# Optimization experiments

Measured on AMD Instinct MI355X. Metric: run time of the kernel, lower is better.

Reference implementation:

```python
import jax, jax.numpy as jnp
import numpy as np

DIM = 256
NUM_HEADS = 8
HEAD_DIM = DIM // NUM_HEADS
CPB_HIDDEN = 512
B, N = 2, 2304
TABLE = 9025  # (2*48-1)**2


def _l2norm(t, eps=1e-12):
    # matches torch F.normalize(dim=-1): x / max(||x||, eps)
    n = jnp.sqrt(jnp.sum(t * t, axis=-1, keepdims=True))
    return t / jnp.maximum(n, eps)


def setup_inputs() -> dict:
    key = jax.random.key(0)
    ks = jax.random.split(key, 12)
    x = jax.random.normal(ks[0], (B, N, DIM), dtype=jnp.float32)
    relative_pos_index = jax.random.randint(ks[1], (N, N), 0, TABLE, dtype=jnp.int64)
    relative_coords_table = jax.random.uniform(ks[2], (TABLE, 2), dtype=jnp.float32) * 2.0 - 1.0
    seq_length_scale = jnp.ones((1,), dtype=jnp.float32) * jnp.log2(jnp.float32(N))
    padding_mask = jnp.zeros((B, N), dtype=jnp.int32)
    s = 0.02
    W_qkv = jax.random.normal(ks[3], (3 * DIM, DIM), dtype=jnp.float32) * s
    b_qkv = jnp.zeros((3 * DIM,), dtype=jnp.float32)
    # temperature init: log(exp(1/0.24) - 1) so softplus(temperature) = 1/0.24
    temperature = jnp.full((NUM_HEADS, 1, 1), float(np.log(np.expm1(1.0 / 0.24))), dtype=jnp.float32)
    query_embedding = jax.random.normal(ks[4], (NUM_HEADS, 1, HEAD_DIM), dtype=jnp.float32) * s
    W_proj = jax.random.normal(ks[5], (DIM, DIM), dtype=jnp.float32) * s
    b_proj = jnp.zeros((DIM,), dtype=jnp.float32)
    W_cpb1 = jax.random.normal(ks[6], (CPB_HIDDEN, 2), dtype=jnp.float32) * s
    b_cpb1 = jnp.zeros((CPB_HIDDEN,), dtype=jnp.float32)
    W_cpb2 = jax.random.normal(ks[7], (NUM_HEADS, CPB_HIDDEN), dtype=jnp.float32) * s
    b_cpb2 = jnp.zeros((NUM_HEADS,), dtype=jnp.float32)
    return {
        'x': x, 'relative_pos_index': relative_pos_index,
        'relative_coords_table': relative_coords_table,
        'seq_length_scale': seq_length_scale, 'padding_mask': padding_mask,
        'W_qkv': W_qkv, 'b_qkv': b_qkv, 'temperature': temperature,
        'query_embedding': query_embedding, 'W_proj': W_proj, 'b_proj': b_proj,
        'W_cpb1': W_cpb1, 'b_cpb1': b_cpb1, 'W_cpb2': W_cpb2, 'b_cpb2': b_cpb2,
    }


def reference(x, relative_pos_index, relative_coords_table, seq_length_scale,
              padding_mask, W_qkv, b_qkv, temperature, query_embedding,
              W_proj, b_proj, W_cpb1, b_cpb1, W_cpb2, b_cpb2):
    Bx, Nx, C = x.shape
    h, d = NUM_HEADS, HEAD_DIM
    # qkv projection -> (B, 3h, N, d); first h heads = q, then k, then v
    qkv = (jnp.einsum('bnc,oc->bno', x, W_qkv) + b_qkv)
    qkv = qkv.reshape(Bx, Nx, 3 * h, d).transpose(0, 2, 1, 3)
    q, k, v = qkv[:, :h], qkv[:, h:2 * h], qkv[:, 2 * h:]
    # CPB relative bias: (T,2) -> (T,h) -> (h,N,N) via gather
    hid = jax.nn.relu(relative_coords_table @ W_cpb1.T + b_cpb1)
    tab = hid @ W_cpb2.T + b_cpb2                    # (T, h)
    rel_bias = tab.T[:, relative_pos_index.reshape(-1)].reshape(h, Nx, Nx)
    # cosine-sim attention with learned query embedding + softplus temperature
    scale = jax.nn.softplus(temperature) * seq_length_scale[0]   # (h,1,1)
    qn = (_l2norm(q) + query_embedding) * scale                  # (B,h,N,d)
    kn = _l2norm(k)
    attn = jnp.einsum('bhnd,bhmd->bhnm', qn, kn) + rel_bias
    attn = jax.nn.softmax(attn, axis=-1)
    out = jnp.einsum('bhnm,bhmd->bhnd', attn, v)
    out = out.transpose(0, 2, 1, 3).reshape(Bx, Nx, C)
    out = out @ W_proj.T + b_proj
    return out
```

## Files before the change

kernel.cpp:

```cpp
#include <hip/hip_runtime.h>
#include <math.h>

#define DIMC 256
#define NHEADS 8
#define HDIM 32
#define CPBH 512
#define BB 2
#define NSEQ 2304
#define TAB 9025
#define TABP 9040
#define RTOT (BB*NHEADS*NSEQ)
#define SPLITS 4
#define MSP (NSEQ/SPLITS)
#define PBS 36
#define NCHUNK (NSEQ/32)
#define LOG2E 1.44269504088896340736f

#define IDXP_ELEMS    (NSEQ * NCHUNK * 16)
#define IDXP4_BLOCKS  (IDXP_ELEMS / 1024)
#define CPB_BLOCKS    ((TAB + 63) / 64)
#define QKV_BLOCKS    (12 * 72)

typedef unsigned short ushort;
typedef __attribute__((ext_vector_type(8))) short short8;
typedef __attribute__((ext_vector_type(4))) short short4v;
typedef __attribute__((ext_vector_type(4))) float f32x4;

#define MFMA16(a,b,c) __builtin_amdgcn_mfma_f32_16x16x32_bf16((a),(b),(c),0,0,0)

#define GL16(SRC, DST) __builtin_amdgcn_global_load_lds( \
    (const __attribute__((address_space(1))) void*)(SRC), \
    (__attribute__((address_space(3))) void*)(DST), 16, 0, 0)

__device__ __forceinline__ ushort f2bf(float x) {
  unsigned u = __float_as_uint(x);
  u += 0x7FFFu + ((u >> 16) & 1u);
  return (ushort)(u >> 16);
}
__device__ __forceinline__ float bf2f(ushort b) {
  return __uint_as_float(((unsigned)b) << 16);
}
__device__ __forceinline__ float fexp2(float x) {
#if defined(__has_builtin)
#if __has_builtin(__builtin_amdgcn_exp2f)
  return __builtin_amdgcn_exp2f(x);
#else
  return exp2f(x);
#endif
#else
  return exp2f(x);
#endif
}
__device__ __forceinline__ unsigned pack_trunc(float p0, float p1) {
  return __builtin_amdgcn_perm(__float_as_uint(p1), __float_as_uint(p0), 0x07060302u);
}
__device__ __forceinline__ void cvt8(const float* __restrict__ p, short8* hi, short8* lo) {
  float4 v0 = *(const float4*)p;
  float4 v1 = *(const float4*)(p + 4);
  float vv[8] = {v0.x, v0.y, v0.z, v0.w, v1.x, v1.y, v1.z, v1.w};
  short8 h, l;
#pragma unroll
  for (int i = 0; i < 8; ++i) {
    ushort hh = f2bf(vv[i]);
    h[i] = (short)hh;
    l[i] = (short)f2bf(vv[i] - bf2f(hh));
  }
  *hi = h; *lo = l;
}

__launch_bounds__(256)
__global__ void pre_kernel(const float* __restrict__ x, const float* __restrict__ wq,
                           const int* __restrict__ idx,
                           const float* __restrict__ tbl, const float* __restrict__ W1,
                           const float* __restrict__ b1, const float* __restrict__ W2,
                           const float* __restrict__ b2,
                           const float* __restrict__ bias, const float* __restrict__ temp,
                           const float* __restrict__ sls, const float* __restrict__ qe,
                           ushort* __restrict__ qhi, ushort* __restrict__ qlo,
                           ushort* __restrict__ khi, ushort* __restrict__ klo,
                           ushort* __restrict__ vT,
                           unsigned* __restrict__ idxP, ushort* __restrict__ tabBf) {
  __shared__ __align__(16) float smem[8192];
  int blk = blockIdx.x;
  int tid = threadIdx.x;

  if (blk < CPB_BLOCKS) {
    float* w1b = smem;
    float* w2t = smem + 2048;
    float* part = smem + 6144;
    for (int i = tid; i < CPBH; i += 256) {
      w1b[i * 4 + 0] = W1[2 * i];
      w1b[i * 4 + 1] = W1[2 * i + 1];
      w1b[i * 4 + 2] = b1[i];
      w1b[i * 4 + 3] = 0.f;
    }
    for (int i = tid; i < CPBH * NHEADS; i += 256)
      w2t[(i & (CPBH - 1)) * NHEADS + (i >> 9)] = W2[i];
    int tl = tid & 63, jc = tid >> 6;
    int t = blk * 64 + tl;
    bool valid = t < TAB;
    float c0 = 0.f, c1 = 0.f;
    if (valid) { c0 = tbl[2 * t]; c1 = tbl[2 * t + 1]; }
    __syncthreads();
    float acc[NHEADS];
#pragma unroll
    for (int h = 0; h < NHEADS; ++h) acc[h] = 0.f;
    for (int j = jc * 128; j < jc * 128 + 128; ++j) {
      float4 wv = *(const float4*)&w1b[j * 4];
      float hid = fmaxf(fmaf(c0, wv.x, fmaf(c1, wv.y, wv.z)), 0.f);
      float4 wa = *(const float4*)&w2t[j * NHEADS];
      float4 wb = *(const float4*)&w2t[j * NHEADS + 4];
      acc[0] = fmaf(hid, wa.x, acc[0]);
      acc[1] = fmaf(hid, wa.y, acc[1]);
      acc[2] = fmaf(hid, wa.z, acc[2]);
      acc[3] = fmaf(hid, wa.w, acc[3]);
      acc[4] = fmaf(hid, wb.x, acc[4]);
      acc[5] = fmaf(hid, wb.y, acc[5]);
      acc[6] = fmaf(hid, wb.z, acc[6]);
      acc[7] = fmaf(hid, wb.w, acc[7]);
    }
#pragma unroll
    for (int h = 0; h < NHEADS; ++h) part[((size_t)jc * 64 + tl) * NHEADS + h] = acc[h];
    __syncthreads();
    if (jc == 0 && valid) {
#pragma unroll
      for (int h = 0; h < NHEADS; ++h) {
        float s = b2[h];
#pragma unroll
        for (int p = 0; p < 4; ++p) s += part[((size_t)p * 64 + tl) * NHEADS + h];
        tabBf[h * TABP + t] = f2bf(s * LOG2E);
      }
    }
  } else if (blk < CPB_BLOCKS + QKV_BLOCKS) {
    float (*vbuf)[65] = (float(*)[65])smem;
    int t = blk - CPB_BLOCKS;
    int n0 = (t % 12) * 64, m0 = (t / 12) * 64;
    int lane = tid & 63, w = tid >> 6;
    int g = lane >> 4, c = lane & 15;
    int mw = m0 + w * 16;
    const int K = DIMC;
    f32x4 acc[4] = {{0,0,0,0},{0,0,0,0},{0,0,0,0},{0,0,0,0}};
#pragma unroll 2
    for (int k0 = 0; k0 < K; k0 += 32) {
      short8 ah, al;
      cvt8(&x[(size_t)(mw + c) * K + k0 + g * 8], &ah, &al);
#pragma unroll
      for (int nt = 0; nt < 4; ++nt) {
        short8 bh, bl;
        cvt8(&wq[(size_t)(n0 + nt * 16 + c) * K + k0 + g * 8], &bh, &bl);
        acc[nt] = MFMA16(ah, bh, acc[nt]);
        acc[nt] = MFMA16(al, bh, acc[nt]);
        acc[nt] = MFMA16(ah, bl, acc[nt]);
      }
    }
#pragma unroll
    for (int nt = 0; nt < 4; ++nt) {
      float bv = bias[n0 + nt * 16 + c];
#pragma unroll
      for (int r = 0; r < 4; ++r) acc[nt][r] += bv;
    }

    int b = (m0 >= NSEQ) ? 1 : 0;
    int nb = m0 - b * NSEQ;
    int sect = n0 >> 8;
    int hloc = (n0 & 255) >> 5;

    if (sect < 2) {
#pragma unroll
      for (int H = 0; H < 2; ++H) {
        int head = hloc + H;
        float scale = (sect == 0) ? log1pf(expf(temp[head])) * sls[0] * LOG2E : 0.f;
#pragma unroll
        for (int r = 0; r < 4; ++r) {
          float ss = acc[2*H][r]*acc[2*H][r] + acc[2*H+1][r]*acc[2*H+1][r];
          ss += __shfl_xor(ss, 1);
          ss += __shfl_xor(ss, 2);
          ss += __shfl_xor(ss, 4);
          ss += __shfl_xor(ss, 8);
          float inv = 1.f / fmaxf(sqrtf(ss), 1e-12f);
#pragma unroll
          for (int half = 0; half < 2; ++half) {
            int d = half * 16 + c;
            float val = acc[2*H + half][r] * inv;
            if (sect == 0) val = (val + qe[head * HDIM + d]) * scale;
            vbuf[w * 16 + g * 4 + r][H * 32 + d] = val;
          }
        }
      }
      __syncthreads();
      int plane = tid >> 7;
      int seg = tid & 127;
      int head = seg >> 6, row = seg & 63;
      const float* srcrow = &vbuf[row][head * 32];
      ushort out16[32];
#pragma unroll
      for (int i = 0; i < 32; ++i) {
        float v = srcrow[i];
        ushort hh = f2bf(v);
        out16[i] = plane ? f2bf(v - bf2f(hh)) : hh;
      }
      ushort* dstp = plane ? (sect == 0 ? qlo : klo) : (sect == 0 ? qhi : khi);
      size_t off = ((size_t)(b * NHEADS + hloc + head) * NSEQ + nb + row) * HDIM;
#pragma unroll
      for (int q4 = 0; q4 < 4; ++q4)
        *(int4*)&dstp[off + q4 * 8] = ((int4*)out16)[q4];
    } else {
#pragma unroll
      for (int nt = 0; nt < 4; ++nt)
#pragma unroll
        for (int r = 0; r < 4; ++r)
          vbuf[w * 16 + g * 4 + r][nt * 16 + c] = acc[nt][r];
      __syncthreads();
      int hbase = (n0 - 512) >> 5;
#pragma unroll
      for (int it = 0; it < 16; ++it) {
        int dloc = (tid >> 6) * 16 + it;
        int p = tid & 63;
        int pp = p & 31;
        int nsrc = (p & 32) + (pp & 1) * 16 + (pp >> 1);
        float v = vbuf[nsrc][dloc];
        int head = hbase + (dloc >> 5), d = dloc & 31;
        vT[((size_t)((b * NHEADS + head) * HDIM + d)) * NSEQ + nb + p] = f2bf(v);
      }
    }
  } else {
    int t4 = (blk - CPB_BLOCKS - QKV_BLOCKS) * 256 + tid;
    int grp = t4 >> 4;
    int ch = grp % NCHUNK;
    int n4 = grp / NCHUNK;
    int m = ch * 32 + (t4 & 15);
    unsigned o[4];
#pragma unroll
    for (int i = 0; i < 4; ++i) {
      unsigned lo = (unsigned)idx[(size_t)(n4 * 4 + i) * NSEQ + m];
      unsigned hi = (unsigned)idx[(size_t)(n4 * 4 + i) * NSEQ + m + 16];
      o[i] = lo | (hi << 16);
    }
    *(uint4*)&idxP[(size_t)t4 * 4] = *(const uint4*)o;
  }
}

__launch_bounds__(256)
__global__ void attn_kernel(const ushort* __restrict__ qhi, const ushort* __restrict__ qlo,
                            const ushort* __restrict__ khi, const ushort* __restrict__ klo,
                            const ushort* __restrict__ vT, const ushort* __restrict__ tabBf,
                            const unsigned* __restrict__ idxP,
                            float* __restrict__ pO, float* __restrict__ pL) {
  __shared__ ushort tbf[10240];
  __shared__ __align__(16) ushort pbuf[8][16 * PBS];
  __shared__ __align__(16) ushort stg[2][6144];
  int tid = threadIdx.x;
  int lane = tid & 63;
  int w = tid >> 6;

  int bid = blockIdx.x;
  int qb = bid >> 5;
  int k8 = bid & 7;
  int j4 = (bid >> 3) & 3;
  int y  = k8 + 8 * j4;
  int s = y & 3, h = y >> 2;

  const ushort* tsrc = tabBf + h * TABP;
#pragma unroll
  for (int i = 0; i < 5; ++i) {
    int off = i * 2048 + tid * 8;
    *(int4*)&tbf[off] = *(const int4*)&tsrc[off];
  }

  int g = lane >> 4, c = lane & 15;
  int q0 = qb * 64 + w * 16;
  int qg0 = q0 >> 2;
  size_t rowA = (size_t)h * NSEQ;
  size_t rowB = (size_t)(NHEADS + h) * NSEQ;
  int m0 = s * MSP;

  int su   = tid & 127;
  int srow = su & 31;
  int sslt = su >> 5;
  const ushort* kb0 = (tid < 128) ? khi : klo;
  const ushort* sA = kb0 + (rowA + m0 + srow) * HDIM + sslt * 8;
  const ushort* sB = kb0 + (rowB + m0 + srow) * HDIM + sslt * 8;
  const ushort* sV = vT + ((size_t)(((tid < 128) ? h : NHEADS + h) * HDIM + srow)) * NSEQ
                     + m0 + sslt * 8;
  unsigned dwb = (unsigned)(tid & 192) * 8;

#define STAGE(DP) do {                         \
    GL16(sA, (DP) + dwb);                      \
    GL16(sB, (DP) + 2048 + dwb);               \
    GL16(sV, (DP) + 4096 + dwb);               \
    sA += 32 * HDIM; sB += 32 * HDIM; sV += 32; \
  } while (0)

  short8 qAh = *(const short8*)&qhi[(rowA + q0 + c) * HDIM + g * 8];
  short8 qAl = *(const short8*)&qlo[(rowA + q0 + c) * HDIM + g * 8];
  short8 qBh = *(const short8*)&qhi[(rowB + q0 + c) * HDIM + g * 8];
  short8 qBl = *(const short8*)&qlo[(rowB + q0 + c) * HDIM + g * 8];

  unsigned oIb = (unsigned)(((unsigned)(qg0 + g) * NCHUNK + (m0 >> 5)) * 64 + c * 4);
  unsigned oI  = oIb;
  uint4 ia = *(const uint4*)&idxP[oI];

  STAGE(&stg[0][0]);
  __syncthreads();

  short one = (c == 0) ? (short)0x3F80 : (short)0;
  short8 onesB = {one, one, one, one, one, one, one, one};

  f32x4 oa0 = {0,0,0,0}, oa1 = {0,0,0,0}, ob0 = {0,0,0,0}, ob1 = {0,0,0,0};
  f32x4 la = {0,0,0,0}, lb = {0,0,0,0};
  ushort* pba = pbuf[w * 2];
  ushort* pbb = pbuf[w * 2 + 1];

  int kbo = g * 256 + c * 8;
  int cur = 0;

  for (int mt = m0; mt < m0 + MSP; mt += 32) {
    bool lastit = (mt + 32 >= m0 + MSP);
    unsigned oIn = lastit ? oIb : oI + 64;
    uint4 ian = *(const uint4*)&idxP[oIn];
    oI = oIn;
    if (!lastit) STAGE(&stg[cur ^ 1][0]);

    const ushort* S = &stg[cur][0];
    short8 ak0h = *(const short8*)&S[kbo];
    short8 ak1h = *(const short8*)&S[kbo + 128];
    short8 ak0l = *(const short8*)&S[1024 + kbo];
    short8 ak1l = *(const short8*)&S[1024 + kbo + 128];
    short8 bk0h = *(const short8*)&S[2048 + kbo];
    short8 bk1h = *(const short8*)&S[2048 + kbo + 128];
    short8 bk0l = *(const short8*)&S[3072 + kbo];
    short8 bk1l = *(const short8*)&S[3072 + kbo + 128];

    f32x4 sa0 = {0,0,0,0}, sa1 = {0,0,0,0}, sb0 = {0,0,0,0}, sb1 = {0,0,0,0};
    sa0 = MFMA16(qAh, ak0h, sa0);
    sa1 = MFMA16(qAh, ak1h, sa1);
    sb0 = MFMA16(qBh, bk0h, sb0);
    sb1 = MFMA16(qBh, bk1h, sb1);
    sa0 = MFMA16(qAl, ak0h, sa0);
    sa1 = MFMA16(qAl, ak1h, sa1);
    sb0 = MFMA16(qBl, bk0h, sb0);
    sb1 = MFMA16(qBl, bk1h, sb1);
    sa0 = MFMA16(qAh, ak0l, sa0);
    sa1 = MFMA16(qAh, ak1l, sa1);
    sb0 = MFMA16(qBh, bk0l, sb0);
    sb1 = MFMA16(qBh, bk1l, sb1);

    unsigned ip[4] = {ia.x, ia.y, ia.z, ia.w};
    float b0[4], b1[4];
#pragma unroll
    for (int r = 0; r < 4; ++r) {
      b0[r] = bf2f(tbf[ip[r] & 0xFFFF]);
      b1[r] = bf2f(tbf[ip[r] >> 16]);
    }
#pragma unroll
    for (int r = 0; r < 4; ++r) {
      float pA0 = fexp2(sa0[r] + b0[r]);
      float pA1 = fexp2(sa1[r] + b1[r]);
      *(unsigned*)&pba[(g * 4 + r) * PBS + 2 * c] = pack_trunc(pA0, pA1);
      float pB0 = fexp2(sb0[r] + b0[r]);
      float pB1 = fexp2(sb1[r] + b1[r]);
      *(unsigned*)&pbb[(g * 4 + r) * PBS + 2 * c] = pack_trunc(pB0, pB1);
    }

    short4v paA = *(const short4v*)&pba[c * PBS + g * 8];
    short4v paB = *(const short4v*)&pba[c * PBS + g * 8 + 4];
    short8 pfa = __builtin_shufflevector(paA, paB, 0, 1, 2, 3, 4, 5, 6, 7);
    short4v pbA = *(const short4v*)&pbb[c * PBS + g * 8];
    short4v pbB = *(const short4v*)&pbb[c * PBS + g * 8 + 4];
    short8 pfb = __builtin_shufflevector(pbA, pbB, 0, 1, 2, 3, 4, 5, 6, 7);

    short8 vf0 = *(const short8*)&S[4096 + kbo];
    short8 vf1 = *(const short8*)&S[4096 + kbo + 128];
    short8 wf0 = *(const short8*)&S[5120 + kbo];
    short8 wf1 = *(const short8*)&S[5120 + kbo + 128];

    oa0 = MFMA16(pfa, vf0, oa0);
    oa1 = MFMA16(pfa, vf1, oa1);
    ob0 = MFMA16(pfb, wf0, ob0);
    ob1 = MFMA16(pfb, wf1, ob1);
    la  = MFMA16(pfa, onesB, la);
    lb  = MFMA16(pfb, onesB, lb);

    ia = ian;
    __syncthreads();
    cur ^= 1;
  }
#undef STAGE

  size_t prowA = (size_t)s * RTOT + rowA;
  size_t prowB = (size_t)s * RTOT + rowB;
#pragma unroll
  for (int r = 0; r < 4; ++r) {
    size_t pra = prowA + q0 + g * 4 + r;
    pO[pra * HDIM + c]      = oa0[r];
    pO[pra * HDIM + 16 + c] = oa1[r];
    size_t prb = prowB + q0 + g * 4 + r;
    pO[prb * HDIM + c]      = ob0[r];
    pO[prb * HDIM + 16 + c] = ob1[r];
    if (c == 0) { pL[pra] = la[r]; pL[prb] = lb[r]; }
  }
}

#define ALD 264
__launch_bounds__(256)
__global__ void gemm_proj_fused(const float* __restrict__ pO, const float* __restrict__ pL,
                                const float* __restrict__ Wp,
                                const float* __restrict__ bias, float* __restrict__ C) {
  __shared__ __align__(16) ushort Ahs[32 * ALD];
  __shared__ __align__(16) ushort Als[32 * ALD];
  int tid = threadIdx.x;
  int m0 = blockIdx.x * 32;
  int b = (m0 >= NSEQ) ? 1 : 0;
  int nb = m0 - b * NSEQ;

  {
    int rr = tid >> 3;
    int q  = tid & 3;
    int hp = (tid >> 2) & 1;
    int n = nb + rr;
#pragma unroll
    for (int hh = 0; hh < 4; ++hh) {
      int h = hp * 4 + hh;
      size_t bhn = (size_t)(b * NHEADS + h) * NSEQ + n;
      float L = 0.f;
#pragma unroll
      for (int sp = 0; sp < SPLITS; ++sp) L += pL[(size_t)sp * RTOT + bhn];
      float inv = 1.f / L;
      float a[8] = {0.f, 0.f, 0.f, 0.f, 0.f, 0.f, 0.f, 0.f};
#pragma unroll
      for (int sp = 0; sp < SPLITS; ++sp) {
        const float* src = &pO[((size_t)sp * RTOT + bhn) * HDIM + q * 8];
        float4 v0 = *(const float4*)&src[0];
        float4 v1 = *(const float4*)&src[4];
        a[0] += v0.x; a[1] += v0.y; a[2] += v0.z; a[3] += v0.w;
        a[4] += v1.x; a[5] += v1.y; a[6] += v1.z; a[7] += v1.w;
      }
      ushort hi8[8], lo8[8];
#pragma unroll
      for (int i = 0; i < 8; ++i) {
        float v = a[i] * inv;
        ushort hh2 = f2bf(v);
        hi8[i] = hh2;
        lo8[i] = f2bf(v - bf2f(hh2));
      }
      int k = h * 32 + q * 8;
      *(int4*)&Ahs[rr * ALD + k] = *(int4*)hi8;
      *(int4*)&Als[rr * ALD + k] = *(int4*)lo8;
    }
  }
  __syncthreads();

  int lane = tid & 63, w = tid >> 6;
  int g = lane >> 4, c = lane & 15;
  int n0 = w * 64;
  f32x4 acc[2][4] = {};
  for (int k0 = 0; k0 < DIMC; k0 += 32) {
    short8 bfh[4], bfl[4];
#pragma unroll
    for (int nt = 0; nt < 4; ++nt)
      cvt8(&Wp[(size_t)(n0 + nt * 16 + c) * DIMC + k0 + g * 8], &bfh[nt], &bfl[nt]);
#pragma unroll
    for (int mt = 0; mt < 2; ++mt) {
      short8 ah = *(const short8*)&Ahs[(mt * 16 + c) * ALD + k0 + g * 8];
      short8 al = *(const short8*)&Als[(mt * 16 + c) * ALD + k0 + g * 8];
#pragma unroll
      for (int nt = 0; nt < 4; ++nt) {
        acc[mt][nt] = MFMA16(ah, bfh[nt], acc[mt][nt]);
        acc[mt][nt] = MFMA16(al, bfh[nt], acc[mt][nt]);
        acc[mt][nt] = MFMA16(ah, bfl[nt], acc[mt][nt]);
      }
    }
  }
#pragma unroll
  for (int nt = 0; nt < 4; ++nt) {
    float bv = bias[n0 + nt * 16 + c];
#pragma unroll
    for (int mt = 0; mt < 2; ++mt)
#pragma unroll
      for (int r = 0; r < 4; ++r)
        C[(size_t)(m0 + mt * 16 + g * 4 + r) * DIMC + n0 + nt * 16 + c] = acc[mt][nt][r] + bv;
  }
}

extern "C" void kernel_launch(void* const* d_in, const int* in_sizes, int n_in,
                              void* d_out, int out_size, void* d_ws, size_t ws_size,
                              hipStream_t stream) {
  const float* x    = (const float*)d_in[0];
  const int*   idx  = (const int*)d_in[1];
  const float* tbl  = (const float*)d_in[2];
  const float* sls  = (const float*)d_in[3];
  const float* Wqkv = (const float*)d_in[5];
  const float* bqkv = (const float*)d_in[6];
  const float* temp = (const float*)d_in[7];
  const float* qe   = (const float*)d_in[8];
  const float* Wp   = (const float*)d_in[9];
  const float* bp   = (const float*)d_in[10];
  const float* W1   = (const float*)d_in[11];
  const float* b1   = (const float*)d_in[12];
  const float* W2   = (const float*)d_in[13];
  const float* b2   = (const float*)d_in[14];

  float* ws   = (float*)d_ws;
  float* pO   = ws;
  float* pL   = pO + (size_t)SPLITS * RTOT * HDIM;
  unsigned* idxP = (unsigned*)(pL + (size_t)SPLITS * RTOT);
  ushort* u   = (ushort*)(idxP + IDXP_ELEMS);
  ushort* qhi = u;                u += (size_t)RTOT * HDIM;
  ushort* qlo = u;                u += (size_t)RTOT * HDIM;
  ushort* khi = u;                u += (size_t)RTOT * HDIM;
  ushort* klo = u;                u += (size_t)RTOT * HDIM;
  ushort* vT  = u;                u += (size_t)RTOT * HDIM;
  ushort* tabBf = u;              u += 73728;
  float* out  = (float*)d_out;

  pre_kernel<<<dim3(CPB_BLOCKS + QKV_BLOCKS + IDXP4_BLOCKS), dim3(256), 0, stream>>>(
      x, Wqkv, idx, tbl, W1, b1, W2, b2, bqkv, temp, sls, qe,
      qhi, qlo, khi, klo, vT, idxP, tabBf);
  attn_kernel<<<dim3((NSEQ / 64) * NHEADS * SPLITS), dim3(256), 0, stream>>>(
      qhi, qlo, khi, klo, vT, tabBf, idxP, pO, pL);
  gemm_proj_fused<<<dim3((BB * NSEQ) / 32), dim3(256), 0, stream>>>(
      pO, pL, Wp, bp, out);
}
```

Before: 206.1 us.

## Stage QKV weight split in LDS, split index packing into own kernel, trim attention LDS

The QKV projection blocks now convert their 64-row slice of W_qkv to bf16 hi/lo once into shared memory, instead of every wave reconverting from global memory on each k-step. The relative-index packing moves into a separate pack_kernel launch, so pre_kernel's shared array can grow to hold the staged weights. In the attention kernel the bias-table LDS buffer shrinks to 9216 entries with a partial final copy, and the P-buffer row stride drops from 36 to 34. Together these cut LDS use to raise occupancy, at the cost of an extra kernel launch and possible bank conflicts from the new strides.

Result: slower. 223.0 us (+8.2%).

```diff
diff --git a/kernel.cpp b/kernel.cpp
--- a/kernel.cpp
+++ b/kernel.cpp
@@ -12,7 +12,7 @@
 #define RTOT (BB*NHEADS*NSEQ)
 #define SPLITS 4
 #define MSP (NSEQ/SPLITS)
-#define PBS 36
+#define PBS 34
 #define NCHUNK (NSEQ/32)
 #define LOG2E 1.44269504088896340736f
 
@@ -69,8 +69,24 @@
 }
 
 __launch_bounds__(256)
+__global__ void pack_kernel(const int* __restrict__ idx, unsigned* __restrict__ idxP) {
+  int t4 = blockIdx.x * 256 + threadIdx.x;
+  int grp = t4 >> 4;
+  int ch = grp % NCHUNK;
+  int n4 = grp / NCHUNK;
+  int m = ch * 32 + (t4 & 15);
+  unsigned o[4];
+#pragma unroll
+  for (int i = 0; i < 4; ++i) {
+    unsigned lo = (unsigned)idx[(size_t)(n4 * 4 + i) * NSEQ + m];
+    unsigned hi = (unsigned)idx[(size_t)(n4 * 4 + i) * NSEQ + m + 16];
+    o[i] = lo | (hi << 16);
+  }
+  *(uint4*)&idxP[(size_t)t4 * 4] = *(const uint4*)o;
+}
+
+__launch_bounds__(256)
 __global__ void pre_kernel(const float* __restrict__ x, const float* __restrict__ wq,
-                           const int* __restrict__ idx,
                            const float* __restrict__ tbl, const float* __restrict__ W1,
                            const float* __restrict__ b1, const float* __restrict__ W2,
                            const float* __restrict__ b2,
@@ -78,13 +94,13 @@
                            const float* __restrict__ sls, const float* __restrict__ qe,
                            ushort* __restrict__ qhi, ushort* __restrict__ qlo,
                            ushort* __restrict__ khi, ushort* __restrict__ klo,
-                           ushort* __restrict__ vT,
-                           unsigned* __restrict__ idxP, ushort* __restrict__ tabBf) {
-  __shared__ __align__(16) float smem[8192];
+                           ushort* __restrict__ vT, ushort* __restrict__ tabBf) {
+  __shared__ __align__(16) ushort smemu[33792];
   int blk = blockIdx.x;
   int tid = threadIdx.x;
 
   if (blk < CPB_BLOCKS) {
+    float* smem = (float*)smemu;
     float* w1b = smem;
     float* w2t = smem + 2048;
     float* part = smem + 6144;
@@ -131,14 +147,29 @@
         tabBf[h * TABP + t] = f2bf(s * LOG2E);
       }
     }
-  } else if (blk < CPB_BLOCKS + QKV_BLOCKS) {
-    float (*vbuf)[65] = (float(*)[65])smem;
+  } else {
+    ushort* bsh = smemu;
+    ushort* bsl = smemu + 64 * 264;
+    float (*vbuf)[65] = (float(*)[65])smemu;
     int t = blk - CPB_BLOCKS;
     int n0 = (t % 12) * 64, m0 = (t / 12) * 64;
     int lane = tid & 63, w = tid >> 6;
     int g = lane >> 4, c = lane & 15;
     int mw = m0 + w * 16;
     const int K = DIMC;
+
+    {
+      int rr = tid >> 2, cq = (tid & 3) * 64;
+#pragma unroll
+      for (int j = 0; j < 64; j += 8) {
+        short8 hh, ll;
+        cvt8(&wq[(size_t)(n0 + rr) * K + cq + j], &hh, &ll);
+        *(short8*)&bsh[rr * 264 + cq + j] = hh;
+        *(short8*)&bsl[rr * 264 + cq + j] = ll;
+      }
+    }
+    __syncthreads();
+
     f32x4 acc[4] = {{0,0,0,0},{0,0,0,0},{0,0,0,0},{0,0,0,0}};
 #pragma unroll 2
     for (int k0 = 0; k0 < K; k0 += 32) {
@@ -146,8 +177,9 @@
       cvt8(&x[(size_t)(mw + c) * K + k0 + g * 8], &ah, &al);
 #pragma unroll
       for (int nt = 0; nt < 4; ++nt) {
-        short8 bh, bl;
-        cvt8(&wq[(size_t)(n0 + nt * 16 + c) * K + k0 + g * 8], &bh, &bl);
+        int br = (nt * 16 + c) * 264 + k0 + g * 8;
+        short8 bh = *(const short8*)&bsh[br];
+        short8 bl = *(const short8*)&bsl[br];
         acc[nt] = MFMA16(ah, bh, acc[nt]);
         acc[nt] = MFMA16(al, bh, acc[nt]);
         acc[nt] = MFMA16(ah, bl, acc[nt]);
@@ -159,6 +191,7 @@
 #pragma unroll
       for (int r = 0; r < 4; ++r) acc[nt][r] += bv;
     }
+    __syncthreads();
 
     int b = (m0 >= NSEQ) ? 1 : 0;
     int nb = m0 - b * NSEQ;
@@ -223,20 +256,6 @@
         vT[((size_t)((b * NHEADS + head) * HDIM + d)) * NSEQ + nb + p] = f2bf(v);
       }
     }
-  } else {
-    int t4 = (blk - CPB_BLOCKS - QKV_BLOCKS) * 256 + tid;
-    int grp = t4 >> 4;
-    int ch = grp % NCHUNK;
-    int n4 = grp / NCHUNK;
-    int m = ch * 32 + (t4 & 15);
-    unsigned o[4];
-#pragma unroll
-    for (int i = 0; i < 4; ++i) {
-      unsigned lo = (unsigned)idx[(size_t)(n4 * 4 + i) * NSEQ + m];
-      unsigned hi = (unsigned)idx[(size_t)(n4 * 4 + i) * NSEQ + m + 16];
-      o[i] = lo | (hi << 16);
-    }
-    *(uint4*)&idxP[(size_t)t4 * 4] = *(const uint4*)o;
   }
 }
 
@@ -246,7 +265,7 @@
                             const ushort* __restrict__ vT, const ushort* __restrict__ tabBf,
                             const unsigned* __restrict__ idxP,
                             float* __restrict__ pO, float* __restrict__ pL) {
-  __shared__ ushort tbf[10240];
+  __shared__ ushort tbf[9216];
   __shared__ __align__(16) ushort pbuf[8][16 * PBS];
   __shared__ __align__(16) ushort stg[2][6144];
   int tid = threadIdx.x;
@@ -262,8 +281,12 @@
 
   const ushort* tsrc = tabBf + h * TABP;
 #pragma unroll
-  for (int i = 0; i < 5; ++i) {
+  for (int i = 0; i < 4; ++i) {
     int off = i * 2048 + tid * 8;
+    *(int4*)&tbf[off] = *(const int4*)&tsrc[off];
+  }
+  if (tid < 128) {
+    int off = 8192 + tid * 8;
     *(int4*)&tbf[off] = *(const int4*)&tsrc[off];
   }
 
@@ -513,9 +536,10 @@
   ushort* tabBf = u;              u += 73728;
   float* out  = (float*)d_out;
 
-  pre_kernel<<<dim3(CPB_BLOCKS + QKV_BLOCKS + IDXP4_BLOCKS), dim3(256), 0, stream>>>(
-      x, Wqkv, idx, tbl, W1, b1, W2, b2, bqkv, temp, sls, qe,
-      qhi, qlo, khi, klo, vT, idxP, tabBf);
+  pack_kernel<<<dim3(IDXP4_BLOCKS), dim3(256), 0, stream>>>(idx, idxP);
+  pre_kernel<<<dim3(CPB_BLOCKS + QKV_BLOCKS), dim3(256), 0, stream>>>(
+      x, Wqkv, tbl, W1, b1, W2, b2, bqkv, temp, sls, qe,
+      qhi, qlo, khi, klo, vT, tabBf);
   attn_kernel<<<dim3((NSEQ / 64) * NHEADS * SPLITS), dim3(256), 0, stream>>>(
       qhi, qlo, khi, klo, vT, tabBf, idxP, pO, pL);
   gemm_proj_fused<<<dim3((BB * NSEQ) / 32), dim3(256), 0, stream>>>(
```
